# Optimization experiments

Measured on AMD Instinct MI355X. Metric: run time of the kernel, lower is better.

The kernel has to match this reference:

```python
import jax, jax.numpy as jnp
import numpy as np

B, S, D, H = 4, 2048, 1024, 16
DK = D // H
NEG = -1.0e9

def setup_inputs() -> dict:
    key = jax.random.key(0)
    ks = jax.random.split(key, 9)
    scale = 1.0 / np.sqrt(D)
    x = jax.random.normal(ks[0], (B, S, D), dtype=jnp.float32)
    # causal mask: positions with mask==0 are filled with -1e9
    mask = jnp.tril(jnp.ones((S, S), dtype=jnp.int32))[None, None]  # [1,1,S,S]
    Wq = jax.random.normal(ks[1], (D, D), dtype=jnp.float32) * scale
    bq = jax.random.normal(ks[2], (D,), dtype=jnp.float32) * 0.01
    Wk = jax.random.normal(ks[3], (D, D), dtype=jnp.float32) * scale
    bk = jax.random.normal(ks[4], (D,), dtype=jnp.float32) * 0.01
    Wv = jax.random.normal(ks[5], (D, D), dtype=jnp.float32) * scale
    bv = jax.random.normal(ks[6], (D,), dtype=jnp.float32) * 0.01
    Wo = jax.random.normal(ks[7], (D, D), dtype=jnp.float32) * scale
    bo = jax.random.normal(ks[8], (D,), dtype=jnp.float32) * 0.01
    return {"x": x, "mask": mask, "Wq": Wq, "bq": bq, "Wk": Wk, "bk": bk,
            "Wv": Wv, "bv": bv, "Wo": Wo, "bo": bo}

def reference(x, mask, Wq, bq, Wk, bk, Wv, bv, Wo, bo):
    Bb, Ss, Dd = x.shape
    q = (x @ Wq.T + bq).reshape(Bb, Ss, H, DK).transpose(0, 2, 1, 3)  # [B,H,S,DK]
    k = (x @ Wk.T + bk).reshape(Bb, Ss, H, DK).transpose(0, 2, 1, 3)
    v = (x @ Wv.T + bv).reshape(Bb, Ss, H, DK).transpose(0, 2, 1, 3)
    scaled = jnp.einsum('bhqd,bhkd->bhqk', q, k) / jnp.sqrt(jnp.float32(DK))
    scaled = jnp.where(mask == 0, jnp.float32(NEG), scaled)
    attn = jax.nn.softmax(scaled, axis=-1)  # dropout prob = 0 -> identity
    vals = jnp.einsum('bhqk,bhkd->bhqd', attn, v)  # [B,H,S,DK]
    vals = vals.transpose(0, 2, 1, 3).reshape(Bb, Ss, H * DK)
    out = vals @ Wo.T + bo
    return out
```

## Files before the change

kernel.cpp:

```cpp
#include <hip/hip_runtime.h>
#include <hip/hip_bf16.h>
#include <cstdint>

#define B_ 4
#define S_ 2048
#define D_ 1024
#define H_ 16
#define DK_ 64

typedef _Float16 h8 __attribute__((ext_vector_type(8)));
typedef _Float16 h4 __attribute__((ext_vector_type(4)));
typedef float f32x4 __attribute__((ext_vector_type(4)));
typedef unsigned int u32x4 __attribute__((ext_vector_type(4)));

__device__ __forceinline__ void gload16(const void* src, void* lds) {
  __builtin_amdgcn_global_load_lds((const __attribute__((address_space(1))) void*)src,
                                   (__attribute__((address_space(3))) void*)lds, 16, 0, 0);
}

__global__ __launch_bounds__(256) void conv_f16(const float* __restrict__ src,
                                                _Float16* __restrict__ dst, int n8) {
  int i = blockIdx.x * 256 + threadIdx.x;
  if (i < n8) {
    int base = i * 8;
    h8 o;
#pragma unroll
    for (int j = 0; j < 8; ++j) o[j] = (_Float16)src[base + j];
    *(h8*)(dst + base) = o;
  }
}

__global__ __launch_bounds__(256) void conv_weights(
    const float* __restrict__ Wq, const float* __restrict__ Wk,
    const float* __restrict__ Wv, const float* __restrict__ Wo,
    const float* __restrict__ bq, const float* __restrict__ bk,
    const float* __restrict__ bv,
    _Float16* __restrict__ wqkv, _Float16* __restrict__ wo,
    float* __restrict__ bqkv) {
  int i = blockIdx.x * 256 + threadIdx.x;
  int seg = i >> 17, r = i & 131071;
  const float* src = seg == 0 ? Wq : seg == 1 ? Wk : seg == 2 ? Wv : Wo;
  int base = r * 8;
  h8 o;
#pragma unroll
  for (int j = 0; j < 8; ++j) o[j] = (_Float16)src[base + j];
  if (seg < 3)
    *(h8*)(wqkv + (size_t)seg * 1048576 + base) = o;
  else
    *(h8*)(wo + base) = o;
  if (i < 768) {
    int bsel = i >> 8, k = (i & 255) * 4;
    const float* bs = bsel == 0 ? bq : bsel == 1 ? bk : bv;
    float4 v = *(const float4*)(bs + k);
    *(float4*)(bqkv + bsel * 1024 + k) = v;
  }
}

__global__ __launch_bounds__(256) void transposeV(const _Float16* __restrict__ V,
                                                  _Float16* __restrict__ Vt) {
  __shared__ unsigned short t[64][72];
  const int bid = blockIdx.x;
  const int bh = bid >> 5, st = bid & 31;
  const int s0 = st * 64;
  const unsigned short* Vb = (const unsigned short*)(V + (size_t)bh * S_ * DK_) + (size_t)s0 * DK_;
  unsigned short* Vtb = (unsigned short*)(Vt + (size_t)bh * DK_ * S_) + s0;
  const int tid = threadIdx.x;
#pragma unroll
  for (int i = 0; i < 16; ++i) {
    int idx = tid + i * 256;
    int r = idx >> 6, cc = idx & 63;
    t[r][cc] = Vb[r * 64 + cc];
  }
  __syncthreads();
#pragma unroll
  for (int i = 0; i < 16; ++i) {
    int idx = tid + i * 256;
    int dk = idx >> 6, sc = idx & 63;
    Vtb[(size_t)dk * S_ + sc] = t[sc][dk];
  }
}

template <int MODE>
__global__ __launch_bounds__(256) void gemm_nt(const _Float16* __restrict__ A,
                                               const _Float16* __restrict__ Bw,
                                               const float* __restrict__ bias,
                                               void* __restrict__ Cout) {
  constexpr int K = D_;
  __shared__ unsigned short lds[2 * 128 * 64];
  char* ldsA = (char*)lds;
  char* ldsB = (char*)(lds + 128 * 64);

  const int tid = threadIdx.x;
  const int w = tid >> 6, lane = tid & 63, g = lane >> 4, c = lane & 15;
  const int wr = w >> 1, wc = w & 1;
  const int bn = blockIdx.x;
  const int bm = blockIdx.y;

  f32x4 acc[4][4] = {};

  const int srow = tid >> 3;
  const int scolsw = ((tid & 7) * 16) ^ ((srow & 7) << 4);
  const char* Ab = (const char*)(A + (size_t)bm * 128 * K);
  const char* Bb = (const char*)(Bw + (size_t)bn * 128 * K);
  const char* Asrc[4];
  const char* Bsrc[4];
#pragma unroll
  for (int j = 0; j < 4; ++j) {
    int row = j * 32 + srow;
    Asrc[j] = Ab + (size_t)row * (K * 2) + scolsw;
    Bsrc[j] = Bb + (size_t)row * (K * 2) + scolsw;
  }
  char* dstA = ldsA + w * 1024;
  char* dstB = ldsB + w * 1024;

  for (int k0 = 0; k0 < K; k0 += 64) {
    __syncthreads();
#pragma unroll
    for (int j = 0; j < 4; ++j) {
      gload16(Asrc[j] + k0 * 2, dstA + j * 4096);
      gload16(Bsrc[j] + k0 * 2, dstB + j * 4096);
    }
    __syncthreads();
#pragma unroll
    for (int kk = 0; kk < 2; ++kk) {
      h8 a[4], b[4];
#pragma unroll
      for (int mi = 0; mi < 4; ++mi) {
        int row = wr * 64 + mi * 16 + c;
        int off = row * 128 + kk * 64 + g * 16;
        a[mi] = *(const h8*)(ldsA + (off ^ ((row & 7) << 4)));
      }
#pragma unroll
      for (int ni = 0; ni < 4; ++ni) {
        int row = wc * 64 + ni * 16 + c;
        int off = row * 128 + kk * 64 + g * 16;
        b[ni] = *(const h8*)(ldsB + (off ^ ((row & 7) << 4)));
      }
#pragma unroll
      for (int mi = 0; mi < 4; ++mi)
#pragma unroll
        for (int ni = 0; ni < 4; ++ni)
          acc[mi][ni] = __builtin_amdgcn_mfma_f32_16x16x32_f16(a[mi], b[ni], acc[mi][ni], 0, 0, 0);
    }
  }

#pragma unroll
  for (int mi = 0; mi < 4; ++mi)
#pragma unroll
    for (int ni = 0; ni < 4; ++ni)
#pragma unroll
      for (int r = 0; r < 4; ++r) {
        int m = bm * 128 + wr * 64 + mi * 16 + g * 4 + r;
        int n = bn * 128 + wc * 64 + ni * 16 + c;
        float v = acc[mi][ni][r] + bias[n];
        if (MODE == 0) {
          int which = n >> 10, nn = n & 1023;
          int bI = m >> 11, sI = m & 2047, hI = nn >> 6, dkI = nn & 63;
          ((_Float16*)Cout)[(size_t)which * 8388608 +
                            (((size_t)bI * H_ + hI) * S_ + sI) * DK_ + dkI] = (_Float16)v;
        } else {
          ((float*)Cout)[(size_t)m * D_ + n] = v;
        }
      }
}

__global__ __launch_bounds__(256) void attn_fwd(const _Float16* __restrict__ Q,
                                                const _Float16* __restrict__ K,
                                                const _Float16* __restrict__ Vt,
                                                _Float16* __restrict__ vals) {
  __shared__ unsigned short ldsK[2 * 64 * 64];
  __shared__ unsigned short ldsV[2 * 64 * 64];
  __shared__ unsigned short ldsP[4 * 16 * 64];
  char* pK = (char*)ldsK;
  char* pV = (char*)ldsV;
  char* pP = (char*)ldsP;

  const int tid = threadIdx.x;
  const int w = tid >> 6, lane = tid & 63, g = lane >> 4, c = lane & 15;
  const int bid = blockIdx.x;
  const int bh = bid >> 4, pi = bid & 15;
  const int bI = bh >> 4, hI = bh & 15;

  const char* Qb = (const char*)(Q + (size_t)bh * S_ * DK_);
  const char* Kb = (const char*)(K + (size_t)bh * S_ * DK_);
  const char* Vtb = (const char*)(Vt + (size_t)bh * DK_ * S_);

  const int srow = tid >> 3;
  const int scol = (tid & 7) * 16;
  int offK[2], offV[2];
#pragma unroll
  for (int j = 0; j < 2; ++j) {
    int row = j * 32 + srow;
    int colsw = scol ^ ((row & 7) << 4);
    offK[j] = row * 128 + colsw;
    offV[j] = row * 4096 + colsw;
  }
  char* dstK = pK + w * 1024;
  char* dstV = pV + w * 1024;

  auto stage = [&](int buf, int kv0) {
#pragma unroll
    for (int j = 0; j < 2; ++j) {
      gload16(Kb + (size_t)kv0 * 128 + offK[j], dstK + buf * 8192 + j * 4096);
      gload16(Vtb + (size_t)kv0 * 2 + offV[j], dstV + buf * 8192 + j * 4096);
    }
  };

  const _Float16 qsc = (_Float16)(0.125f * 1.44269504f);

  for (int phase = 0; phase < 2; ++phase) {
    const int qsub = (phase == 0) ? pi : 31 - pi;
    const int qw0 = qsub * 64 + w * 16;

    h8 qf[2];
#pragma unroll
    for (int kk = 0; kk < 2; ++kk) {
      h8 v = *(const h8*)(Qb + (size_t)(qw0 + c) * 128 + kk * 64 + g * 16);
#pragma unroll
      for (int j = 0; j < 8; ++j) v[j] *= qsc;
      qf[kk] = v;
    }

    f32x4 o[4] = {};
    float m_ = -1e30f, l_ = 0.f;

    const int ntile = qsub + 1;
    stage(0, 0);
    __syncthreads();

    for (int t = 0; t < ntile; ++t) {
      const int cur = t & 1;
      if (t + 1 < ntile) stage(cur ^ 1, (t + 1) * 64);
      const char* bK = pK + cur * 8192;
      const char* bV = pV + cur * 8192;

      f32x4 s[4] = {};
#pragma unroll
      for (int kk = 0; kk < 2; ++kk) {
        h8 kf[4];
#pragma unroll
        for (int ni = 0; ni < 4; ++ni) {
          int row = ni * 16 + c;
          int off = row * 128 + kk * 64 + g * 16;
          kf[ni] = *(const h8*)(bK + (off ^ ((c & 7) << 4)));
        }
#pragma unroll
        for (int ni = 0; ni < 4; ++ni)
          s[ni] = __builtin_amdgcn_mfma_f32_16x16x32_f16(kf[ni], qf[kk], s[ni], 0, 0, 0);
      }

      if (t == ntile - 1) {
#pragma unroll
        for (int ni = 0; ni < 4; ++ni)
#pragma unroll
          for (int r = 0; r < 4; ++r) {
            int kv = ni * 16 + g * 4 + r;
            int q = w * 16 + c;
            if (kv > q) s[ni][r] = -1e30f;
          }
      }

      float tm = s[0][0];
#pragma unroll
      for (int ni = 0; ni < 4; ++ni)
#pragma unroll
        for (int r = 0; r < 4; ++r) tm = fmaxf(tm, s[ni][r]);
      tm = fmaxf(tm, __shfl_xor(tm, 16));
      tm = fmaxf(tm, __shfl_xor(tm, 32));

      const bool noresc = __all(tm <= m_ + 8.f);
      const float mn = noresc ? m_ : fmaxf(m_, tm);

      float rs = 0.f;
      float p[4][4];
#pragma unroll
      for (int ni = 0; ni < 4; ++ni)
#pragma unroll
        for (int r = 0; r < 4; ++r) {
          float e = __builtin_amdgcn_exp2f(s[ni][r] - mn);
          p[ni][r] = e;
          rs += e;
        }
      rs += __shfl_xor(rs, 16);
      rs += __shfl_xor(rs, 32);

      if (noresc) {
        l_ += rs;
      } else {
        float al = __builtin_amdgcn_exp2f(m_ - mn);
        l_ = l_ * al + rs;
        m_ = mn;
#pragma unroll
        for (int r = 0; r < 4; ++r) {
          float alr = __shfl(al, g * 4 + r);
#pragma unroll
          for (int nd = 0; nd < 4; ++nd) o[nd][r] *= alr;
        }
      }

#pragma unroll
      for (int ni = 0; ni < 4; ++ni) {
        h4 pk4 = {(_Float16)p[ni][0], (_Float16)p[ni][1], (_Float16)p[ni][2], (_Float16)p[ni][3]};
        int off = w * 2048 + c * 128 + ni * 32 + g * 8;
        *(h4*)(pP + (off ^ ((c & 7) << 4))) = pk4;
      }

#pragma unroll
      for (int kk = 0; kk < 2; ++kk) {
        h8 pf, vf[4];
        {
          int off = w * 2048 + c * 128 + kk * 64 + g * 16;
          pf = *(const h8*)(pP + (off ^ ((c & 7) << 4)));
        }
#pragma unroll
        for (int nd = 0; nd < 4; ++nd) {
          int row = nd * 16 + c;
          int off = row * 128 + kk * 64 + g * 16;
          vf[nd] = *(const h8*)(bV + (off ^ ((c & 7) << 4)));
        }
#pragma unroll
        for (int nd = 0; nd < 4; ++nd)
          o[nd] = __builtin_amdgcn_mfma_f32_16x16x32_f16(pf, vf[nd], o[nd], 0, 0, 0);
      }

      __syncthreads();
    }

#pragma unroll
    for (int r = 0; r < 4; ++r) {
      float lr = __shfl(l_, g * 4 + r);
      float inv = 1.0f / lr;
      int qrow = qsub * 64 + w * 16 + g * 4 + r;
#pragma unroll
      for (int nd = 0; nd < 4; ++nd) {
        int col = hI * 64 + nd * 16 + c;
        vals[((size_t)bI * S_ + qrow) * D_ + col] = (_Float16)(o[nd][r] * inv);
      }
    }
  }
}

extern "C" void kernel_launch(void* const* d_in, const int* in_sizes, int n_in,
                              void* d_out, int out_size, void* d_ws, size_t ws_size,
                              hipStream_t stream) {
  const float* x  = (const float*)d_in[0];
  const float* Wq = (const float*)d_in[2];
  const float* bq = (const float*)d_in[3];
  const float* Wk = (const float*)d_in[4];
  const float* bk = (const float*)d_in[5];
  const float* Wv = (const float*)d_in[6];
  const float* bv = (const float*)d_in[7];
  const float* Wo = (const float*)d_in[8];
  const float* bo = (const float*)d_in[9];
  float* out = (float*)d_out;

  char* ws = (char*)d_ws;
  size_t off = 0;
  auto alloc = [&](size_t bytes) {
    char* p = ws + off;
    off += (bytes + 255) & ~(size_t)255;
    return p;
  };
  _Float16* xb   = (_Float16*)alloc((size_t)B_ * S_ * D_ * 2);
  _Float16* wqkv = (_Float16*)alloc((size_t)3 * D_ * D_ * 2);
  _Float16* wob  = (_Float16*)alloc((size_t)D_ * D_ * 2);
  float*    bqkv = (float*)alloc((size_t)3 * D_ * 4);
  _Float16* qkvw = (_Float16*)alloc((size_t)3 * B_ * H_ * S_ * DK_ * 2);
  _Float16* Vtw  = (_Float16*)alloc((size_t)B_ * H_ * S_ * DK_ * 2);
  _Float16* valw = (_Float16*)alloc((size_t)B_ * S_ * D_ * 2);

  const int nx8 = B_ * S_ * D_ / 8;
  conv_f16<<<(nx8 + 255) / 256, 256, 0, stream>>>(x, xb, nx8);
  conv_weights<<<2048, 256, 0, stream>>>(Wq, Wk, Wv, Wo, bq, bk, bv, wqkv, wob, bqkv);

  gemm_nt<0><<<dim3(24, 64), 256, 0, stream>>>(xb, wqkv, bqkv, qkvw);

  transposeV<<<B_ * H_ * (S_ / 64), 256, 0, stream>>>(qkvw + (size_t)2 * 8388608, Vtw);

  attn_fwd<<<1024, 256, 0, stream>>>(qkvw, qkvw + (size_t)8388608, Vtw, valw);

  gemm_nt<1><<<dim3(8, 64), 256, 0, stream>>>(valw, wob, bo, out);
}
```

Measured before the change: 202.9 us.

## Fuse V transpose into QKV GEMM epilogue and interleave two causal query tiles

The QKV GEMM now writes the V projection directly in transposed layout, so the separate transposeV kernel and its round trip through memory go away. The attention kernel processes its two query tiles (short and long) in one K/V loop, so each staged K/V tile is shared by both groups instead of being loaded twice. Block indexing is remapped so neighbouring blocks cover different heads. The change also adds s_setprio around MFMA blocks, a launch-bounds occupancy hint, a cheaper online-softmax rescale check, and packed fp16 conversion. The cost is higher register pressure from holding two sets of accumulators, plus scattered 8-byte stores in the V epilogue.

```diff
diff --git a/kernel.cpp b/kernel.cpp
--- a/kernel.cpp
+++ b/kernel.cpp
@@ -10,6 +10,7 @@
 
 typedef _Float16 h8 __attribute__((ext_vector_type(8)));
 typedef _Float16 h4 __attribute__((ext_vector_type(4)));
+typedef _Float16 h2 __attribute__((ext_vector_type(2)));
 typedef float f32x4 __attribute__((ext_vector_type(4)));
 typedef unsigned int u32x4 __attribute__((ext_vector_type(4)));
 
@@ -56,35 +57,12 @@
   }
 }
 
-__global__ __launch_bounds__(256) void transposeV(const _Float16* __restrict__ V,
-                                                  _Float16* __restrict__ Vt) {
-  __shared__ unsigned short t[64][72];
-  const int bid = blockIdx.x;
-  const int bh = bid >> 5, st = bid & 31;
-  const int s0 = st * 64;
-  const unsigned short* Vb = (const unsigned short*)(V + (size_t)bh * S_ * DK_) + (size_t)s0 * DK_;
-  unsigned short* Vtb = (unsigned short*)(Vt + (size_t)bh * DK_ * S_) + s0;
-  const int tid = threadIdx.x;
-#pragma unroll
-  for (int i = 0; i < 16; ++i) {
-    int idx = tid + i * 256;
-    int r = idx >> 6, cc = idx & 63;
-    t[r][cc] = Vb[r * 64 + cc];
-  }
-  __syncthreads();
-#pragma unroll
-  for (int i = 0; i < 16; ++i) {
-    int idx = tid + i * 256;
-    int dk = idx >> 6, sc = idx & 63;
-    Vtb[(size_t)dk * S_ + sc] = t[sc][dk];
-  }
-}
-
 template <int MODE>
 __global__ __launch_bounds__(256) void gemm_nt(const _Float16* __restrict__ A,
                                                const _Float16* __restrict__ Bw,
                                                const float* __restrict__ bias,
-                                               void* __restrict__ Cout) {
+                                               void* __restrict__ Cout,
+                                               _Float16* __restrict__ Vt) {
   constexpr int K = D_;
   __shared__ unsigned short lds[2 * 128 * 64];
   char* ldsA = (char*)lds;
@@ -136,38 +114,57 @@
         int off = row * 128 + kk * 64 + g * 16;
         b[ni] = *(const h8*)(ldsB + (off ^ ((row & 7) << 4)));
       }
+      __builtin_amdgcn_s_setprio(1);
 #pragma unroll
       for (int mi = 0; mi < 4; ++mi)
 #pragma unroll
         for (int ni = 0; ni < 4; ++ni)
           acc[mi][ni] = __builtin_amdgcn_mfma_f32_16x16x32_f16(a[mi], b[ni], acc[mi][ni], 0, 0, 0);
-    }
-  }
-
-#pragma unroll
-  for (int mi = 0; mi < 4; ++mi)
-#pragma unroll
-    for (int ni = 0; ni < 4; ++ni)
-#pragma unroll
-      for (int r = 0; r < 4; ++r) {
-        int m = bm * 128 + wr * 64 + mi * 16 + g * 4 + r;
+      __builtin_amdgcn_s_setprio(0);
+    }
+  }
+
+  if (MODE == 0 && bn >= 16) {
+#pragma unroll
+    for (int mi = 0; mi < 4; ++mi)
+#pragma unroll
+      for (int ni = 0; ni < 4; ++ni) {
+        int m0 = bm * 128 + wr * 64 + mi * 16 + g * 4;
         int n = bn * 128 + wc * 64 + ni * 16 + c;
-        float v = acc[mi][ni][r] + bias[n];
-        if (MODE == 0) {
-          int which = n >> 10, nn = n & 1023;
-          int bI = m >> 11, sI = m & 2047, hI = nn >> 6, dkI = nn & 63;
-          ((_Float16*)Cout)[(size_t)which * 8388608 +
-                            (((size_t)bI * H_ + hI) * S_ + sI) * DK_ + dkI] = (_Float16)v;
-        } else {
-          ((float*)Cout)[(size_t)m * D_ + n] = v;
+        float bb = bias[n];
+        h4 v4;
+#pragma unroll
+        for (int r = 0; r < 4; ++r) v4[r] = (_Float16)(acc[mi][ni][r] + bb);
+        int bI = m0 >> 11, sI = m0 & 2047;
+        int dk = n & 63, hh = (n >> 6) & 15;
+        *(h4*)(Vt + (((size_t)(bI * 16 + hh) * 64 + dk) * 2048 + sI)) = v4;
+      }
+  } else {
+#pragma unroll
+    for (int mi = 0; mi < 4; ++mi)
+#pragma unroll
+      for (int ni = 0; ni < 4; ++ni)
+#pragma unroll
+        for (int r = 0; r < 4; ++r) {
+          int m = bm * 128 + wr * 64 + mi * 16 + g * 4 + r;
+          int n = bn * 128 + wc * 64 + ni * 16 + c;
+          float v = acc[mi][ni][r] + bias[n];
+          if (MODE == 0) {
+            int which = n >> 10, nn = n & 1023;
+            int bI = m >> 11, sI = m & 2047, hI = nn >> 6, dkI = nn & 63;
+            ((_Float16*)Cout)[(size_t)which * 8388608 +
+                              (((size_t)bI * H_ + hI) * S_ + sI) * DK_ + dkI] = (_Float16)v;
+          } else {
+            ((float*)Cout)[(size_t)m * D_ + n] = v;
+          }
         }
-      }
-}
-
-__global__ __launch_bounds__(256) void attn_fwd(const _Float16* __restrict__ Q,
-                                                const _Float16* __restrict__ K,
-                                                const _Float16* __restrict__ Vt,
-                                                _Float16* __restrict__ vals) {
+  }
+}
+
+__global__ __launch_bounds__(256, 4) void attn_fwd(const _Float16* __restrict__ Q,
+                                                   const _Float16* __restrict__ K,
+                                                   const _Float16* __restrict__ Vt,
+                                                   _Float16* __restrict__ vals) {
   __shared__ unsigned short ldsK[2 * 64 * 64];
   __shared__ unsigned short ldsV[2 * 64 * 64];
   __shared__ unsigned short ldsP[4 * 16 * 64];
@@ -178,8 +175,10 @@
   const int tid = threadIdx.x;
   const int w = tid >> 6, lane = tid & 63, g = lane >> 4, c = lane & 15;
   const int bid = blockIdx.x;
-  const int bh = bid >> 4, pi = bid & 15;
+  const int pi = bid >> 6;
+  const int bh = bid & 63;
   const int bI = bh >> 4, hI = bh & 15;
+  const int q0 = pi, q1 = 31 - pi;
 
   const char* Qb = (const char*)(Q + (size_t)bh * S_ * DK_);
   const char* Kb = (const char*)(K + (size_t)bh * S_ * DK_);
@@ -207,137 +206,142 @@
   };
 
   const _Float16 qsc = (_Float16)(0.125f * 1.44269504f);
-
-  for (int phase = 0; phase < 2; ++phase) {
-    const int qsub = (phase == 0) ? pi : 31 - pi;
-    const int qw0 = qsub * 64 + w * 16;
-
-    h8 qf[2];
+  h8 qf[2][2];
+#pragma unroll
+  for (int gi = 0; gi < 2; ++gi) {
+    int qsub = gi ? q1 : q0;
+    int qr = qsub * 64 + w * 16 + c;
 #pragma unroll
     for (int kk = 0; kk < 2; ++kk) {
-      h8 v = *(const h8*)(Qb + (size_t)(qw0 + c) * 128 + kk * 64 + g * 16);
+      h8 v = *(const h8*)(Qb + (size_t)qr * 128 + kk * 64 + g * 16);
 #pragma unroll
       for (int j = 0; j < 8; ++j) v[j] *= qsc;
-      qf[kk] = v;
-    }
-
-    f32x4 o[4] = {};
-    float m_ = -1e30f, l_ = 0.f;
-
-    const int ntile = qsub + 1;
-    stage(0, 0);
-    __syncthreads();
-
-    for (int t = 0; t < ntile; ++t) {
-      const int cur = t & 1;
-      if (t + 1 < ntile) stage(cur ^ 1, (t + 1) * 64);
-      const char* bK = pK + cur * 8192;
-      const char* bV = pV + cur * 8192;
-
-      f32x4 s[4] = {};
-#pragma unroll
-      for (int kk = 0; kk < 2; ++kk) {
-        h8 kf[4];
-#pragma unroll
-        for (int ni = 0; ni < 4; ++ni) {
-          int row = ni * 16 + c;
-          int off = row * 128 + kk * 64 + g * 16;
-          kf[ni] = *(const h8*)(bK + (off ^ ((c & 7) << 4)));
-        }
+      qf[gi][kk] = v;
+    }
+  }
+
+  f32x4 o0[4] = {}, o1[4] = {};
+  float m0v = -1e30f, l0v = 0.f, m1v = -1e30f, l1v = 0.f;
+
+  const int nt = q1 + 1;
+  stage(0, 0);
+  __syncthreads();
+
+  const int sw = (c & 7) << 4;
+
+  for (int t = 0; t < nt; ++t) {
+    const int cur = t & 1;
+    if (t + 1 < nt) stage(cur ^ 1, (t + 1) * 64);
+    const char* bK = pK + cur * 8192;
+    const char* bV = pV + cur * 8192;
+    const bool g0on = (t <= q0);
+
+    f32x4 s0[4] = {}, s1[4] = {};
+#pragma unroll
+    for (int kk = 0; kk < 2; ++kk) {
+      h8 kfx[4];
+#pragma unroll
+      for (int ni = 0; ni < 4; ++ni) {
+        int row = ni * 16 + c;
+        kfx[ni] = *(const h8*)(bK + ((row * 128 + kk * 64 + g * 16) ^ sw));
+      }
+      __builtin_amdgcn_s_setprio(1);
+#pragma unroll
+      for (int ni = 0; ni < 4; ++ni)
+        s1[ni] = __builtin_amdgcn_mfma_f32_16x16x32_f16(kfx[ni], qf[1][kk], s1[ni], 0, 0, 0);
+      if (g0on)
 #pragma unroll
         for (int ni = 0; ni < 4; ++ni)
-          s[ni] = __builtin_amdgcn_mfma_f32_16x16x32_f16(kf[ni], qf[kk], s[ni], 0, 0, 0);
-      }
-
-      if (t == ntile - 1) {
+          s0[ni] = __builtin_amdgcn_mfma_f32_16x16x32_f16(kfx[ni], qf[0][kk], s0[ni], 0, 0, 0);
+      __builtin_amdgcn_s_setprio(0);
+    }
+
+    auto dogroup = [&](f32x4(&s)[4], f32x4(&og)[4], float& mm, float& ll, bool diag) {
+      if (diag) {
 #pragma unroll
         for (int ni = 0; ni < 4; ++ni)
 #pragma unroll
           for (int r = 0; r < 4; ++r) {
             int kv = ni * 16 + g * 4 + r;
-            int q = w * 16 + c;
-            if (kv > q) s[ni][r] = -1e30f;
+            if (kv > w * 16 + c) s[ni][r] = -1e30f;
           }
       }
-
-      float tm = s[0][0];
+      float m4[4];
 #pragma unroll
       for (int ni = 0; ni < 4; ++ni)
-#pragma unroll
-        for (int r = 0; r < 4; ++r) tm = fmaxf(tm, s[ni][r]);
-      tm = fmaxf(tm, __shfl_xor(tm, 16));
-      tm = fmaxf(tm, __shfl_xor(tm, 32));
-
-      const bool noresc = __all(tm <= m_ + 8.f);
-      const float mn = noresc ? m_ : fmaxf(m_, tm);
-
-      float rs = 0.f;
-      float p[4][4];
-#pragma unroll
-      for (int ni = 0; ni < 4; ++ni)
-#pragma unroll
-        for (int r = 0; r < 4; ++r) {
-          float e = __builtin_amdgcn_exp2f(s[ni][r] - mn);
-          p[ni][r] = e;
-          rs += e;
-        }
-      rs += __shfl_xor(rs, 16);
-      rs += __shfl_xor(rs, 32);
-
-      if (noresc) {
-        l_ += rs;
-      } else {
-        float al = __builtin_amdgcn_exp2f(m_ - mn);
-        l_ = l_ * al + rs;
-        m_ = mn;
+        m4[ni] = fmaxf(fmaxf(s[ni][0], s[ni][1]), fmaxf(s[ni][2], s[ni][3]));
+      float pmax = fmaxf(fmaxf(m4[0], m4[1]), fmaxf(m4[2], m4[3]));
+      if (!__all(pmax <= mm + 8.f)) {
+        float rm = fmaxf(pmax, __shfl_xor(pmax, 16));
+        rm = fmaxf(rm, __shfl_xor(rm, 32));
+        float mn = fmaxf(mm, rm);
+        float al = __builtin_amdgcn_exp2f(mm - mn);
+        mm = mn;
+        ll *= al;
 #pragma unroll
         for (int r = 0; r < 4; ++r) {
           float alr = __shfl(al, g * 4 + r);
 #pragma unroll
-          for (int nd = 0; nd < 4; ++nd) o[nd][r] *= alr;
+          for (int nd = 0; nd < 4; ++nd) og[nd][r] *= alr;
         }
       }
-
+      const float mn = mm;
+      float rs = 0.f;
 #pragma unroll
       for (int ni = 0; ni < 4; ++ni) {
-        h4 pk4 = {(_Float16)p[ni][0], (_Float16)p[ni][1], (_Float16)p[ni][2], (_Float16)p[ni][3]};
+        float e0 = __builtin_amdgcn_exp2f(s[ni][0] - mn);
+        float e1 = __builtin_amdgcn_exp2f(s[ni][1] - mn);
+        float e2 = __builtin_amdgcn_exp2f(s[ni][2] - mn);
+        float e3 = __builtin_amdgcn_exp2f(s[ni][3] - mn);
+        rs += (e0 + e1) + (e2 + e3);
+        h2 lo = __builtin_bit_cast(h2, __builtin_amdgcn_cvt_pkrtz(e0, e1));
+        h2 hi = __builtin_bit_cast(h2, __builtin_amdgcn_cvt_pkrtz(e2, e3));
+        h4 pk4 = {lo[0], lo[1], hi[0], hi[1]};
         int off = w * 2048 + c * 128 + ni * 32 + g * 8;
-        *(h4*)(pP + (off ^ ((c & 7) << 4))) = pk4;
-      }
+        *(h4*)(pP + (off ^ sw)) = pk4;
+      }
+      ll += rs;
 
 #pragma unroll
       for (int kk = 0; kk < 2; ++kk) {
-        h8 pf, vf[4];
-        {
-          int off = w * 2048 + c * 128 + kk * 64 + g * 16;
-          pf = *(const h8*)(pP + (off ^ ((c & 7) << 4)));
-        }
+        h8 pf = *(const h8*)(pP + ((w * 2048 + c * 128 + kk * 64 + g * 16) ^ sw));
+        h8 vf[4];
 #pragma unroll
         for (int nd = 0; nd < 4; ++nd) {
           int row = nd * 16 + c;
-          int off = row * 128 + kk * 64 + g * 16;
-          vf[nd] = *(const h8*)(bV + (off ^ ((c & 7) << 4)));
+          vf[nd] = *(const h8*)(bV + ((row * 128 + kk * 64 + g * 16) ^ sw));
         }
+        __builtin_amdgcn_s_setprio(1);
 #pragma unroll
         for (int nd = 0; nd < 4; ++nd)
-          o[nd] = __builtin_amdgcn_mfma_f32_16x16x32_f16(pf, vf[nd], o[nd], 0, 0, 0);
-      }
-
-      __syncthreads();
-    }
-
+          og[nd] = __builtin_amdgcn_mfma_f32_16x16x32_f16(pf, vf[nd], og[nd], 0, 0, 0);
+        __builtin_amdgcn_s_setprio(0);
+      }
+    };
+
+    if (g0on) dogroup(s0, o0, m0v, l0v, t == q0);
+    dogroup(s1, o1, m1v, l1v, t == q1);
+
+    __syncthreads();
+  }
+
+  auto epi = [&](f32x4(&og)[4], float ll, int qsub) {
+    float lt = ll + __shfl_xor(ll, 16);
+    lt += __shfl_xor(lt, 32);
+    float linv = 1.0f / lt;
 #pragma unroll
     for (int r = 0; r < 4; ++r) {
-      float lr = __shfl(l_, g * 4 + r);
-      float inv = 1.0f / lr;
+      float inv = __shfl(linv, g * 4 + r);
       int qrow = qsub * 64 + w * 16 + g * 4 + r;
 #pragma unroll
       for (int nd = 0; nd < 4; ++nd) {
         int col = hI * 64 + nd * 16 + c;
-        vals[((size_t)bI * S_ + qrow) * D_ + col] = (_Float16)(o[nd][r] * inv);
-      }
-    }
-  }
+        vals[((size_t)bI * S_ + qrow) * D_ + col] = (_Float16)(og[nd][r] * inv);
+      }
+    }
+  };
+  epi(o0, l0v, q0);
+  epi(o1, l1v, q1);
 }
 
 extern "C" void kernel_launch(void* const* d_in, const int* in_sizes, int n_in,
@@ -365,7 +369,7 @@
   _Float16* wqkv = (_Float16*)alloc((size_t)3 * D_ * D_ * 2);
   _Float16* wob  = (_Float16*)alloc((size_t)D_ * D_ * 2);
   float*    bqkv = (float*)alloc((size_t)3 * D_ * 4);
-  _Float16* qkvw = (_Float16*)alloc((size_t)3 * B_ * H_ * S_ * DK_ * 2);
+  _Float16* qkvw = (_Float16*)alloc((size_t)2 * B_ * H_ * S_ * DK_ * 2);
   _Float16* Vtw  = (_Float16*)alloc((size_t)B_ * H_ * S_ * DK_ * 2);
   _Float16* valw = (_Float16*)alloc((size_t)B_ * S_ * D_ * 2);
 
@@ -373,11 +377,9 @@
   conv_f16<<<(nx8 + 255) / 256, 256, 0, stream>>>(x, xb, nx8);
   conv_weights<<<2048, 256, 0, stream>>>(Wq, Wk, Wv, Wo, bq, bk, bv, wqkv, wob, bqkv);
 
-  gemm_nt<0><<<dim3(24, 64), 256, 0, stream>>>(xb, wqkv, bqkv, qkvw);
-
-  transposeV<<<B_ * H_ * (S_ / 64), 256, 0, stream>>>(qkvw + (size_t)2 * 8388608, Vtw);
+  gemm_nt<0><<<dim3(24, 64), 256, 0, stream>>>(xb, wqkv, bqkv, qkvw, Vtw);
 
   attn_fwd<<<1024, 256, 0, stream>>>(qkvw, qkvw + (size_t)8388608, Vtw, valw);
 
-  gemm_nt<1><<<dim3(8, 64), 256, 0, stream>>>(valw, wob, bo, out);
-}
+  gemm_nt<1><<<dim3(8, 64), 256, 0, stream>>>(valw, wob, bo, out, nullptr);
+}
```

After: 194.7 us. -4.1%, faster.
